# Kernel tuning notes

Hardware: AMD Instinct MI355X
Metric: run time of the kernel (lower is better)

## Reference

```python
import jax, jax.numpy as jnp
import numpy as np

B, S, H = 2, 2048, 1024
NH, HD = 16, 64


def setup_inputs() -> dict:
    key = jax.random.key(0)
    ks = jax.random.split(key, 6)
    sc = 0.02
    return {
        "hidden_states": jax.random.normal(ks[0], (B, S, H), dtype=jnp.float32),
        "attention_mask": jnp.zeros((B, 1, 1, S), dtype=jnp.float32),
        "rel_pos": jax.random.normal(ks[1], (B, NH, S, S), dtype=jnp.float32) * 0.1,
        "Wq": jax.random.normal(ks[2], (H, H), dtype=jnp.float32) * sc,
        "bq": jnp.zeros((H,), dtype=jnp.float32),
        "Wk": jax.random.normal(ks[3], (H, H), dtype=jnp.float32) * sc,
        "bk": jnp.zeros((H,), dtype=jnp.float32),
        "Wv": jax.random.normal(ks[4], (H, H), dtype=jnp.float32) * sc,
        "bv": jnp.zeros((H,), dtype=jnp.float32),
    }


def reference(hidden_states, attention_mask, rel_pos, Wq, bq, Wk, bk, Wv, bv):
    def heads(x):  # [B,S,H] -> [B,NH,S,HD]
        return x.reshape(B, S, NH, HD).transpose(0, 2, 1, 3)

    q = heads(hidden_states @ Wq.T + bq)
    k = heads(hidden_states @ Wk.T + bk)
    v = heads(hidden_states @ Wv.T + bv)

    scores = jnp.einsum('bhqd,bhkd->bhqk', q, k) / jnp.sqrt(jnp.float32(HD))
    scores = scores + attention_mask + rel_pos
    probs = jax.nn.softmax(scores, axis=-1)
    ctx = jnp.einsum('bhqk,bhkd->bhqd', probs, v)
    return ctx.transpose(0, 2, 1, 3).reshape(B, S, H)
```

## Files before the change

kernel.cpp:

```cpp
#include <hip/hip_runtime.h>
#include <hip/hip_bf16.h>

#define B_  2
#define S_  2048
#define H_  1024
#define NH_ 16
#define HD_ 64

typedef __bf16 bf16_t;
typedef __attribute__((ext_vector_type(4))) __bf16 bf16x4;
typedef __attribute__((ext_vector_type(8))) __bf16 bf16x8;
typedef __attribute__((ext_vector_type(4))) float f32x4;

__device__ __forceinline__ void gld_lds16(const bf16_t* g, bf16_t* l) {
    __builtin_amdgcn_global_load_lds(
        (const __attribute__((address_space(1))) unsigned int*)g,
        (__attribute__((address_space(3))) unsigned int*)l, 16, 0, 0);
}

__global__ __launch_bounds__(256) void cast_bf16(
    const float* __restrict__ X, const float* __restrict__ Wq,
    const float* __restrict__ Wk, const float* __restrict__ Wv,
    bf16_t* __restrict__ Xb, bf16_t* __restrict__ Wb)
{
    const size_t XN = (size_t)B_ * S_ * H_;
    size_t i4 = ((size_t)blockIdx.x * 256 + threadIdx.x) * 4;
    const float* src;
    bf16_t* dst;
    if (i4 < XN) {
        src = X + i4; dst = Xb + i4;
    } else {
        size_t j = i4 - XN;
        int wsel = (int)(j >> 20);
        const float* Wp = wsel == 0 ? Wq : (wsel == 1 ? Wk : Wv);
        src = Wp + (j & 1048575); dst = Wb + j;
    }
    float4 v = *(const float4*)src;
    bf16x4 o = { (bf16_t)v.x, (bf16_t)v.y, (bf16_t)v.z, (bf16_t)v.w };
    *(bf16x4*)dst = o;
}

__global__ __launch_bounds__(256) void qkv_gemm(
    const bf16_t* __restrict__ Xb, const bf16_t* __restrict__ Wb,
    const float* __restrict__ bq, const float* __restrict__ bk,
    const float* __restrict__ bv,
    bf16_t* __restrict__ qbuf, bf16_t* __restrict__ kbuf, bf16_t* __restrict__ vbuf)
{
    const int which = blockIdx.z;
    const bf16_t* W  = Wb + (size_t)which * H_ * H_;
    const float* bias = which == 0 ? bq : (which == 1 ? bk : bv);
    bf16_t* out       = which == 0 ? qbuf : (which == 1 ? kbuf : vbuf);
    const float scale = which == 0 ? 0.125f : 1.0f;

    const int m0 = blockIdx.x * 128;
    const int n0 = blockIdx.y * 128;
    const int t    = threadIdx.x;
    const int lane = t & 63;
    const int w    = t >> 6;
    const int wr   = w >> 1, wc = w & 1;
    const int lo   = lane & 15, g = lane >> 4;

    __shared__ bf16_t As[128 * 64];
    __shared__ bf16_t Bs[128 * 64];

    const int srow = w * 8 + (lane >> 3);
    const int scol = (lane & 7) * 8;
    const bf16_t* ga = Xb + (size_t)(m0 + srow) * H_ + scol;
    const bf16_t* gb = W  + (size_t)(n0 + srow) * H_ + scol;

    f32x4 acc[4][4];
#pragma unroll
    for (int mt = 0; mt < 4; ++mt)
#pragma unroll
        for (int nt = 0; nt < 4; ++nt)
            acc[mt][nt] = (f32x4){0.f, 0.f, 0.f, 0.f};

    for (int kc = 0; kc < 16; ++kc) {
#pragma unroll
        for (int p = 0; p < 4; ++p) {
            gld_lds16(ga + (size_t)p * 32 * H_ + kc * 64, &As[p * 2048 + w * 512]);
            gld_lds16(gb + (size_t)p * 32 * H_ + kc * 64, &Bs[p * 2048 + w * 512]);
        }
        __syncthreads();

        bf16x8 a0[4], a1[4];
#pragma unroll
        for (int mt = 0; mt < 4; ++mt) {
            a0[mt] = *(const bf16x8*)&As[(wr * 64 + mt * 16 + lo) * 64 + g * 8];
            a1[mt] = *(const bf16x8*)&As[(wr * 64 + mt * 16 + lo) * 64 + g * 8 + 32];
        }
#pragma unroll
        for (int nt = 0; nt < 4; ++nt) {
            bf16x8 b0 = *(const bf16x8*)&Bs[(wc * 64 + nt * 16 + lo) * 64 + g * 8];
            bf16x8 b1 = *(const bf16x8*)&Bs[(wc * 64 + nt * 16 + lo) * 64 + g * 8 + 32];
#pragma unroll
            for (int mt = 0; mt < 4; ++mt) {
                acc[mt][nt] = __builtin_amdgcn_mfma_f32_16x16x32_bf16(a0[mt], b0, acc[mt][nt], 0, 0, 0);
                acc[mt][nt] = __builtin_amdgcn_mfma_f32_16x16x32_bf16(a1[mt], b1, acc[mt][nt], 0, 0, 0);
            }
        }
        __syncthreads();
    }

#pragma unroll
    for (int nt = 0; nt < 4; ++nt) {
        int n  = n0 + wc * 64 + nt * 16 + lo;
        int hh = n >> 6, d = n & 63;
        float bv_ = bias[n];
#pragma unroll
        for (int mt = 0; mt < 4; ++mt) {
#pragma unroll
            for (int r = 0; r < 4; ++r) {
                int m = m0 + wr * 64 + mt * 16 + g * 4 + r;
                int b = m >> 11, s = m & 2047;
                out[(((size_t)(b * NH_ + hh) * S_) + s) * HD_ + d] =
                    (bf16_t)((acc[mt][nt][r] + bv_) * scale);
            }
        }
    }
}

__global__ __launch_bounds__(256, 4) void attn(
    const bf16_t* __restrict__ qbuf, const bf16_t* __restrict__ kbuf,
    const bf16_t* __restrict__ vbuf,
    const float* __restrict__ mask, const float* __restrict__ rel,
    float* __restrict__ out)
{
    const int b = blockIdx.z, h = blockIdx.y, q0 = blockIdx.x * 64;
    const int t    = threadIdx.x;
    const int lane = t & 63;
    const int w    = t >> 6;
    const int lo   = lane & 15;
    const int g    = lane >> 4;

    __shared__ bf16_t QPs[64 * 72];
    __shared__ bf16_t Ks[64 * 72];
    __shared__ bf16_t VTs[64 * 72];

    const bf16_t* qg = qbuf + ((size_t)(b * NH_ + h) * S_ + q0) * HD_;
    const bf16_t* kg = kbuf + (size_t)(b * NH_ + h) * S_ * HD_;
    const bf16_t* vg = vbuf + (size_t)(b * NH_ + h) * S_ * HD_;
    const float*  relg  = rel + ((size_t)((b * NH_ + h) * S_ + q0)) * S_;
    const float*  maskg = mask + b * S_;

#pragma unroll
    for (int p = 0; p < 2; ++p) {
        int idx = t + p * 256;
        int row = idx >> 3, c8 = (idx & 7) * 8;
        *(uint4*)&QPs[row * 72 + c8] = *(const uint4*)&qg[row * 64 + c8];
    }
    __syncthreads();

    bf16x8 aq0 = *(const bf16x8*)&QPs[(w * 16 + lo) * 72 + g * 8];
    bf16x8 aq1 = *(const bf16x8*)&QPs[(w * 16 + lo) * 72 + g * 8 + 32];

    float mi[4], li[4];
    f32x4 accO[4];
#pragma unroll
    for (int r = 0; r < 4; ++r) { mi[r] = -1e30f; li[r] = 0.f; }
#pragma unroll
    for (int dt = 0; dt < 4; ++dt) accO[dt] = (f32x4){0.f, 0.f, 0.f, 0.f};

    const int qrow = w * 16 + g * 4;

    float rl[4][4];
#pragma unroll
    for (int r = 0; r < 4; ++r)
#pragma unroll
        for (int nt = 0; nt < 4; ++nt)
            rl[r][nt] = relg[(size_t)(qrow + r) * S_ + nt * 16 + lo];

    for (int kc = 0; kc < 32; ++kc) {
#pragma unroll
        for (int p = 0; p < 2; ++p) {
            int idx = t + p * 256;
            int row = idx >> 3, c8 = (idx & 7) * 8;
            *(uint4*)&Ks[row * 72 + c8] = *(const uint4*)&kg[(size_t)(kc * 64 + row) * 64 + c8];
            uint4 vv = *(const uint4*)&vg[(size_t)(kc * 64 + row) * 64 + c8];
            const bf16_t* vvp = (const bf16_t*)&vv;
            int sw = row ^ c8;
#pragma unroll
            for (int j = 0; j < 8; ++j) VTs[(c8 + j) * 72 + sw] = vvp[j];
        }
        __syncthreads();

        f32x4 sc[4];
#pragma unroll
        for (int nt = 0; nt < 4; ++nt) {
            bf16x8 b0 = *(const bf16x8*)&Ks[(nt * 16 + lo) * 72 + g * 8];
            bf16x8 b1 = *(const bf16x8*)&Ks[(nt * 16 + lo) * 72 + g * 8 + 32];
            f32x4 z = (f32x4){0.f, 0.f, 0.f, 0.f};
            z = __builtin_amdgcn_mfma_f32_16x16x32_bf16(aq0, b0, z, 0, 0, 0);
            z = __builtin_amdgcn_mfma_f32_16x16x32_bf16(aq1, b1, z, 0, 0, 0);
            sc[nt] = z;
        }

        float sv[4][4];
#pragma unroll
        for (int nt = 0; nt < 4; ++nt) {
            float mk = maskg[kc * 64 + nt * 16 + lo];
#pragma unroll
            for (int r = 0; r < 4; ++r)
                sv[r][nt] = sc[nt][r] + mk + rl[r][nt];
        }

        if (kc < 31) {
#pragma unroll
            for (int r = 0; r < 4; ++r)
#pragma unroll
                for (int nt = 0; nt < 4; ++nt)
                    rl[r][nt] = relg[(size_t)(qrow + r) * S_ + (kc + 1) * 64 + nt * 16 + lo];
        }

        bf16_t* Pw = &QPs[w * 16 * 72];
#pragma unroll
        for (int r = 0; r < 4; ++r) {
            float vmax = fmaxf(fmaxf(sv[r][0], sv[r][1]), fmaxf(sv[r][2], sv[r][3]));
#pragma unroll
            for (int mk2 = 1; mk2 < 16; mk2 <<= 1)
                vmax = fmaxf(vmax, __shfl_xor(vmax, mk2, 16));
            float mnew  = fmaxf(mi[r], vmax);
            float alpha = __expf(mi[r] - mnew);
            float rsum = 0.f;
#pragma unroll
            for (int nt = 0; nt < 4; ++nt) {
                float p = __expf(sv[r][nt] - mnew);
                sv[r][nt] = p;
                rsum += p;
            }
#pragma unroll
            for (int mk2 = 1; mk2 < 16; mk2 <<= 1)
                rsum += __shfl_xor(rsum, mk2, 16);
            li[r] = li[r] * alpha + rsum;
            mi[r] = mnew;
#pragma unroll
            for (int dt = 0; dt < 4; ++dt) accO[dt][r] *= alpha;
#pragma unroll
            for (int nt = 0; nt < 4; ++nt)
                Pw[(g * 4 + r) * 72 + ((nt * 16 + lo) ^ (g * 8))] = (bf16_t)sv[r][nt];
        }

        bf16x8 pa0 = *(const bf16x8*)&Pw[lo * 72 + ((g * 8)       ^ ((lo >> 2) * 8))];
        bf16x8 pa1 = *(const bf16x8*)&Pw[lo * 72 + (((4 + g) * 8) ^ ((lo >> 2) * 8))];
#pragma unroll
        for (int dt = 0; dt < 4; ++dt) {
            int d = dt * 16 + lo;
            bf16x8 v0 = *(const bf16x8*)&VTs[d * 72 + ((g * 8)       ^ (d & 56))];
            bf16x8 v1 = *(const bf16x8*)&VTs[d * 72 + (((4 + g) * 8) ^ (d & 56))];
            accO[dt] = __builtin_amdgcn_mfma_f32_16x16x32_bf16(pa0, v0, accO[dt], 0, 0, 0);
            accO[dt] = __builtin_amdgcn_mfma_f32_16x16x32_bf16(pa1, v1, accO[dt], 0, 0, 0);
        }
        __syncthreads();
    }

#pragma unroll
    for (int dt = 0; dt < 4; ++dt) {
        int d = dt * 16 + lo;
#pragma unroll
        for (int r = 0; r < 4; ++r) {
            int row = q0 + w * 16 + g * 4 + r;
            out[((size_t)(b * S_ + row)) * H_ + h * HD_ + d] = accO[dt][r] / li[r];
        }
    }
}

extern "C" void kernel_launch(void* const* d_in, const int* in_sizes, int n_in,
                              void* d_out, int out_size, void* d_ws, size_t ws_size,
                              hipStream_t stream) {
    const float* hs   = (const float*)d_in[0];
    const float* mask = (const float*)d_in[1];
    const float* rel  = (const float*)d_in[2];
    const float* Wq   = (const float*)d_in[3];
    const float* bq   = (const float*)d_in[4];
    const float* Wk   = (const float*)d_in[5];
    const float* bk   = (const float*)d_in[6];
    const float* Wv   = (const float*)d_in[7];
    const float* bv   = (const float*)d_in[8];
    float* out = (float*)d_out;

    const size_t qkv_elems = (size_t)B_ * NH_ * S_ * HD_;
    bf16_t* qbuf = (bf16_t*)d_ws;
    bf16_t* kbuf = qbuf + qkv_elems;
    bf16_t* vbuf = kbuf + qkv_elems;
    bf16_t* Xb   = vbuf + qkv_elems;
    bf16_t* Wb   = Xb   + qkv_elems;

    cast_bf16<<<7168, 256, 0, stream>>>(hs, Wq, Wk, Wv, Xb, Wb);
    qkv_gemm<<<dim3(32, 8, 3), 256, 0, stream>>>(Xb, Wb, bq, bk, bv,
                                                 qbuf, kbuf, vbuf);
    attn<<<dim3(S_ / 64, NH_, B_), 256, 0, stream>>>(qbuf, kbuf, vbuf, mask, rel, out);
}
```

Baseline: 827.7 us.

## Register-prefetch next K/V tile, cache mask in LDS, remap blocks for XCD locality

The attention kernel now loads the next K/V tile into registers while the current tile is being computed, so global latency overlaps with the MFMA work. The mask is staged once into shared memory instead of being read from global memory every iteration. Blocks are remapped with a 1D grid so that blocks sharing the same head land on the same XCD, and MFMA sections are wrapped in s_setprio. Launch bounds drop to 3 waves per SIMD to make room for the extra registers, at the cost of lower occupancy. The barrier at the end of the loop no longer waits for memory counters.

```diff
diff --git a/kernel.cpp b/kernel.cpp
--- a/kernel.cpp
+++ b/kernel.cpp
@@ -120,13 +120,18 @@
     }
 }
 
-__global__ __launch_bounds__(256, 4) void attn(
+__global__ __launch_bounds__(256, 3) void attn(
     const bf16_t* __restrict__ qbuf, const bf16_t* __restrict__ kbuf,
     const bf16_t* __restrict__ vbuf,
     const float* __restrict__ mask, const float* __restrict__ rel,
     float* __restrict__ out)
 {
-    const int b = blockIdx.z, h = blockIdx.y, q0 = blockIdx.x * 64;
+    const int bid  = blockIdx.x;
+    const int work = ((bid & 7) << 7) | (bid >> 3);
+    const int q0 = (work & 31) * 64;
+    const int h  = (work >> 5) & 15;
+    const int b  = work >> 9;
+
     const int t    = threadIdx.x;
     const int lane = t & 63;
     const int w    = t >> 6;
@@ -134,22 +139,44 @@
     const int g    = lane >> 4;
 
     __shared__ bf16_t QPs[64 * 72];
-    __shared__ bf16_t Ks[64 * 72];
+    __shared__ bf16_t Ks [64 * 72];
     __shared__ bf16_t VTs[64 * 72];
+    __shared__ float  Ms [S_];
 
     const bf16_t* qg = qbuf + ((size_t)(b * NH_ + h) * S_ + q0) * HD_;
     const bf16_t* kg = kbuf + (size_t)(b * NH_ + h) * S_ * HD_;
     const bf16_t* vg = vbuf + (size_t)(b * NH_ + h) * S_ * HD_;
     const float*  relg  = rel + ((size_t)((b * NH_ + h) * S_ + q0)) * S_;
-    const float*  maskg = mask + b * S_;
-
-#pragma unroll
-    for (int p = 0; p < 2; ++p) {
-        int idx = t + p * 256;
-        int row = idx >> 3, c8 = (idx & 7) * 8;
-        *(uint4*)&QPs[row * 72 + c8] = *(const uint4*)&qg[row * 64 + c8];
-    }
-    __syncthreads();
+    const float*  maskg = mask + (size_t)b * S_;
+
+    const int r0 = t >> 3;
+    const int c8 = (t & 7) * 8;
+
+    uint4 kv0 = *(const uint4*)&kg[(size_t)r0 * 64 + c8];
+    uint4 kv1 = *(const uint4*)&kg[(size_t)(r0 + 32) * 64 + c8];
+    uint4 vv0 = *(const uint4*)&vg[(size_t)r0 * 64 + c8];
+    uint4 vv1 = *(const uint4*)&vg[(size_t)(r0 + 32) * 64 + c8];
+
+    uint4  qv0 = *(const uint4*)&qg[(size_t)r0 * 64 + c8];
+    uint4  qv1 = *(const uint4*)&qg[(size_t)(r0 + 32) * 64 + c8];
+    float4 mv0 = *(const float4*)&maskg[t * 8];
+    float4 mv1 = *(const float4*)&maskg[t * 8 + 4];
+
+    const int qrow = w * 16 + g * 4;
+    float rl[4][4];
+#pragma unroll
+    for (int r = 0; r < 4; ++r)
+#pragma unroll
+        for (int nt = 0; nt < 4; ++nt)
+            rl[r][nt] = relg[(size_t)(qrow + r) * S_ + nt * 16 + lo];
+
+    *(uint4*)&QPs[r0 * 72 + c8]        = qv0;
+    *(uint4*)&QPs[(r0 + 32) * 72 + c8] = qv1;
+    *(float4*)&Ms[t * 8]     = mv0;
+    *(float4*)&Ms[t * 8 + 4] = mv1;
+
+    asm volatile("s_waitcnt lgkmcnt(0)" ::: "memory");
+    __builtin_amdgcn_s_barrier();
 
     bf16x8 aq0 = *(const bf16x8*)&QPs[(w * 16 + lo) * 72 + g * 8];
     bf16x8 aq1 = *(const bf16x8*)&QPs[(w * 16 + lo) * 72 + g * 8 + 32];
@@ -161,30 +188,34 @@
 #pragma unroll
     for (int dt = 0; dt < 4; ++dt) accO[dt] = (f32x4){0.f, 0.f, 0.f, 0.f};
 
-    const int qrow = w * 16 + g * 4;
-
-    float rl[4][4];
-#pragma unroll
-    for (int r = 0; r < 4; ++r)
-#pragma unroll
-        for (int nt = 0; nt < 4; ++nt)
-            rl[r][nt] = relg[(size_t)(qrow + r) * S_ + nt * 16 + lo];
-
     for (int kc = 0; kc < 32; ++kc) {
-#pragma unroll
-        for (int p = 0; p < 2; ++p) {
-            int idx = t + p * 256;
-            int row = idx >> 3, c8 = (idx & 7) * 8;
-            *(uint4*)&Ks[row * 72 + c8] = *(const uint4*)&kg[(size_t)(kc * 64 + row) * 64 + c8];
-            uint4 vv = *(const uint4*)&vg[(size_t)(kc * 64 + row) * 64 + c8];
-            const bf16_t* vvp = (const bf16_t*)&vv;
-            int sw = row ^ c8;
-#pragma unroll
-            for (int j = 0; j < 8; ++j) VTs[(c8 + j) * 72 + sw] = vvp[j];
-        }
-        __syncthreads();
+        *(uint4*)&Ks[r0 * 72 + c8]        = kv0;
+        *(uint4*)&Ks[(r0 + 32) * 72 + c8] = kv1;
+        {
+            const bf16_t* vp0 = (const bf16_t*)&vv0;
+            const bf16_t* vp1 = (const bf16_t*)&vv1;
+            int sw0 = r0 ^ c8, sw1 = (r0 + 32) ^ c8;
+#pragma unroll
+            for (int j = 0; j < 8; ++j) {
+                VTs[(c8 + j) * 72 + sw0] = vp0[j];
+                VTs[(c8 + j) * 72 + sw1] = vp1[j];
+            }
+        }
+        {
+            const int kn = (kc < 31) ? kc + 1 : kc;
+            const bf16_t* kgn = kg + (size_t)kn * 64 * 64;
+            const bf16_t* vgn = vg + (size_t)kn * 64 * 64;
+            kv0 = *(const uint4*)&kgn[(size_t)r0 * 64 + c8];
+            kv1 = *(const uint4*)&kgn[(size_t)(r0 + 32) * 64 + c8];
+            vv0 = *(const uint4*)&vgn[(size_t)r0 * 64 + c8];
+            vv1 = *(const uint4*)&vgn[(size_t)(r0 + 32) * 64 + c8];
+        }
+
+        asm volatile("s_waitcnt lgkmcnt(0)" ::: "memory");
+        __builtin_amdgcn_s_barrier();
 
         f32x4 sc[4];
+        __builtin_amdgcn_s_setprio(1);
 #pragma unroll
         for (int nt = 0; nt < 4; ++nt) {
             bf16x8 b0 = *(const bf16x8*)&Ks[(nt * 16 + lo) * 72 + g * 8];
@@ -194,11 +225,12 @@
             z = __builtin_amdgcn_mfma_f32_16x16x32_bf16(aq1, b1, z, 0, 0, 0);
             sc[nt] = z;
         }
+        __builtin_amdgcn_s_setprio(0);
 
         float sv[4][4];
 #pragma unroll
         for (int nt = 0; nt < 4; ++nt) {
-            float mk = maskg[kc * 64 + nt * 16 + lo];
+            float mk = Ms[kc * 64 + nt * 16 + lo];
 #pragma unroll
             for (int r = 0; r < 4; ++r)
                 sv[r][nt] = sc[nt][r] + mk + rl[r][nt];
@@ -242,6 +274,7 @@
 
         bf16x8 pa0 = *(const bf16x8*)&Pw[lo * 72 + ((g * 8)       ^ ((lo >> 2) * 8))];
         bf16x8 pa1 = *(const bf16x8*)&Pw[lo * 72 + (((4 + g) * 8) ^ ((lo >> 2) * 8))];
+        __builtin_amdgcn_s_setprio(1);
 #pragma unroll
         for (int dt = 0; dt < 4; ++dt) {
             int d = dt * 16 + lo;
@@ -250,7 +283,9 @@
             accO[dt] = __builtin_amdgcn_mfma_f32_16x16x32_bf16(pa0, v0, accO[dt], 0, 0, 0);
             accO[dt] = __builtin_amdgcn_mfma_f32_16x16x32_bf16(pa1, v1, accO[dt], 0, 0, 0);
         }
-        __syncthreads();
+        __builtin_amdgcn_s_setprio(0);
+
+        __builtin_amdgcn_s_barrier();
     }
 
 #pragma unroll
@@ -288,5 +323,5 @@
     cast_bf16<<<7168, 256, 0, stream>>>(hs, Wq, Wk, Wv, Xb, Wb);
     qkv_gemm<<<dim3(32, 8, 3), 256, 0, stream>>>(Xb, Wb, bq, bk, bv,
                                                  qbuf, kbuf, vbuf);
-    attn<<<dim3(S_ / 64, NH_, B_), 256, 0, stream>>>(qbuf, kbuf, vbuf, mask, rel, out);
-}
+    attn<<<1024, 256, 0, stream>>>(qbuf, kbuf, vbuf, mask, rel, out);
+}
```

Result: faster. 795.7 us (-3.9%).
